# Kernel tuning notes

Hardware: AMD Instinct MI355X
Metric: run time of the kernel (lower is better)

## Reference

```python
import jax, jax.numpy as jnp
import numpy as np

CHUNK = 64
EPS = 1e-5


def segsum(a):
    # a: (..., T) -> (..., T, T) lower-triangular cumulative segment sums; -inf above diag
    T = a.shape[-1]
    cs = jnp.cumsum(a, axis=-1)
    ss = cs[..., :, None] - cs[..., None, :]
    mask = jnp.tril(jnp.ones((T, T), dtype=bool))
    return jnp.where(mask, ss, -jnp.inf)


def ssd(x, A, B, C, chunk):
    # x: (b, L, h, p), A: (b, L, h), B/C: (b, L, n)
    b, L, h, p = x.shape
    c = L // chunk
    x = x.reshape(b, c, chunk, h, p)
    A = A.reshape(b, c, chunk, h).transpose(0, 3, 1, 2)          # b h c l
    B = B.reshape(b, c, chunk, -1)                               # b c l n
    C = C.reshape(b, c, chunk, -1)                               # b c l n
    A_cum = jnp.cumsum(A, axis=-1)                               # b h c l
    Lmat = jnp.exp(segsum(A))                                    # b h c l l (causal decay)
    # intra-chunk (diagonal-block) output
    Y_diag = jnp.einsum('bcln,bcsn,bhcls,bcshp->bclhp', C, B, Lmat, x)
    # per-chunk states
    decay_states = jnp.exp(A_cum[..., -1:] - A_cum)              # b h c l
    states = jnp.einsum('bcln,bhcl,bclhp->bchpn', B, decay_states, x)
    states = jnp.concatenate([jnp.zeros_like(states[:, :1]), states], axis=1)  # b (c+1) h p n
    # inter-chunk recurrence via chunk-level segsum
    A_last = jnp.pad(A_cum[..., -1], ((0, 0), (0, 0), (1, 0)))   # b h (c+1)
    decay_chunk = jnp.exp(segsum(A_last))                        # b h (c+1) (c+1)
    new_states = jnp.einsum('bhzc,bchpn->bzhpn', decay_chunk, states)
    states, final = new_states[:, :-1], new_states[:, -1:]
    Y_off = jnp.einsum('bcln,bchpn,bhcl->bclhp', C, states, jnp.exp(A_cum))
    return (Y_diag + Y_off).reshape(b, L, h, p), final


def mamba2(x, W_in, conv_w, conv_b, dt_bias, A_log, D, norm_w, W_out):
    d_inner = norm_w.shape[0]
    nheads = dt_bias.shape[0]
    d_state = (conv_b.shape[0] - d_inner) // 2
    headdim = d_inner // nheads
    k_conv = conv_w.shape[0]
    b, L, _ = x.shape

    zxbcdt = x @ W_in                                            # (b, L, 2*d_inner+2*n+h)
    z = zxbcdt[..., :d_inner]
    xBC = zxbcdt[..., d_inner:2 * d_inner + 2 * d_state]
    dt = jax.nn.softplus(zxbcdt[..., 2 * d_inner + 2 * d_state:] + dt_bias)  # (b, L, h)
    A = -jnp.exp(A_log)                                          # (h,)

    # causal depthwise conv (zero init conv state == left-pad k_conv-1 zeros) + silu
    xp = jnp.pad(xBC, ((0, 0), (k_conv - 1, 0), (0, 0)))
    xBC = jax.lax.conv_general_dilated(
        xp, conv_w, (1,), 'VALID',
        dimension_numbers=('NWC', 'WIO', 'NWC'),
        feature_group_count=conv_b.shape[0])
    xBC = jax.nn.silu(xBC + conv_b)

    xs = xBC[..., :d_inner].reshape(b, L, nheads, headdim)       # (b, L, h, p)
    Bm = xBC[..., d_inner:d_inner + d_state]                     # (b, L, n)
    Cm = xBC[..., d_inner + d_state:]                            # (b, L, n)

    Y, _ = ssd(xs * dt[..., None], A * dt, Bm, Cm, CHUNK)
    Y = Y + xs * D                                               # D: (h, 1) broadcasts over p
    y = Y.reshape(b, L, d_inner)

    # gated RMSNorm
    y = y * jax.nn.silu(z)
    y = y * jax.lax.rsqrt(jnp.mean(y * y, axis=-1, keepdims=True) + EPS) * norm_w
    return y @ W_out


def setup_inputs():
    key = jax.random.key(0)
    ks = jax.random.split(key, 8)
    B, L, d_model = 2, 4096, 1024
    expand, d_state, k_conv, headdim = 2, 128, 4, 64
    d_inner = expand * d_model
    nheads = d_inner // headdim
    d_in_proj = 2 * d_inner + 2 * d_state + nheads
    conv_dim = d_inner + 2 * d_state
    return {
        'x': jax.random.normal(ks[0], (B, L, d_model), jnp.float32),
        'W_in': jax.random.normal(ks[1], (d_model, d_in_proj), jnp.float32) / np.sqrt(d_model).astype(np.float32),
        'conv_w': jax.random.normal(ks[2], (k_conv, 1, conv_dim), jnp.float32) / np.sqrt(k_conv).astype(np.float32),
        'conv_b': jnp.zeros((conv_dim,), jnp.float32),
        'dt_bias': jax.random.normal(ks[3], (nheads,), jnp.float32) * 0.5 - 2.0,
        'A_log': jnp.log(1.0 + 15.0 * jax.random.uniform(ks[4], (nheads,), jnp.float32)),
        'D': jax.random.normal(ks[5], (nheads, 1), jnp.float32),
        'norm_w': jnp.ones((d_inner,), jnp.float32),
        'W_out': jax.random.normal(ks[6], (d_inner, d_model), jnp.float32) / np.sqrt(d_inner).astype(np.float32),
    }


def reference(x, W_in, conv_w, conv_b, dt_bias, A_log, D, norm_w, W_out):
    return mamba2(x, W_in, conv_w, conv_b, dt_bias, A_log, D, norm_w, W_out)
```

## Files before the change

kernel.cpp:

```cpp
#include <hip/hip_runtime.h>
#include <hip/hip_fp16.h>

typedef _Float16 f16;
typedef _Float16 f16x4 __attribute__((ext_vector_type(4)));
typedef _Float16 f16x8 __attribute__((ext_vector_type(8)));
typedef float f32x4 __attribute__((ext_vector_type(4)));

#define DEV __device__ __forceinline__

constexpr int BB    = 2;
constexpr int LL    = 4096;
constexpr int DM    = 1024;
constexpr int DIN   = 2048;
constexpr int DST   = 128;
constexpr int NH    = 32;
constexpr int HD    = 64;
constexpr int NC    = 64;
constexpr int MROWS = BB * LL;
constexpr int NPROJ = 2*DIN + 2*DST + NH;
constexpr int NZ    = 2*DIN + 2*DST;
constexpr int CONVD = DIN + 2*DST;
constexpr int DT_OFF = 2*DIN + 2*DST;
constexpr int BOFF  = DIN;
constexpr int COFF  = DIN + DST;

DEV float silu_f(float v) { return v / (1.f + __expf(-v)); }

DEV void gload_lds16(const f16* gsrc, f16* lds_dst) {
  __builtin_amdgcn_global_load_lds(
      (const __attribute__((address_space(1))) void*)gsrc,
      (__attribute__((address_space(3))) void*)lds_dst, 16, 0, 0);
}

__global__ __launch_bounds__(256)
void tof16_kernel(const float* __restrict__ src, f16* __restrict__ dst, int n8) {
  int i = blockIdx.x * 256 + threadIdx.x;
  if (i >= n8) return;
  f32x4 a = *(const f32x4*)(src + (size_t)i*8);
  f32x4 b = *(const f32x4*)(src + (size_t)i*8 + 4);
  f16x8 o;
#pragma unroll
  for (int j = 0; j < 4; ++j) { o[j] = (f16)a[j]; o[4+j] = (f16)b[j]; }
  *(f16x8*)(dst + (size_t)i*8) = o;
}

__global__ __launch_bounds__(256)
void transpose_f32_to_f16(const float* __restrict__ src, f16* __restrict__ dst,
                          int K, int N, int srcLd) {
  __shared__ float tbuf[32][33];
  int n0 = blockIdx.x * 32, k0 = blockIdx.y * 32;
  int tx = threadIdx.x & 31, ty = threadIdx.x >> 5;
  for (int i = ty; i < 32; i += 8)
    tbuf[i][tx] = src[(size_t)(k0 + i)*srcLd + n0 + tx];
  __syncthreads();
  for (int i = ty; i < 32; i += 8)
    dst[(size_t)(n0 + i)*K + (k0 + tx)] = (f16)tbuf[tx][i];
}

template<bool C16>
__global__ __launch_bounds__(256)
void gemm_lds(const f16* __restrict__ A, const f16* __restrict__ Bt,
              void* __restrict__ Cp, int M, int N, int K, int ldc) {
  __shared__ f16 As[128*64];
  __shared__ f16 Bs[128*64];
  int nbn = N >> 7;
  int bm = blockIdx.x / nbn, bn = blockIdx.x % nbn;
  const int tid  = threadIdx.x;
  const int wave = tid >> 6, lane = tid & 63;
  const int lrow = lane & 15;
  const int kgrp = lane >> 4;
  const int wr = wave >> 1, wc = wave & 1;
  const int srow = lane >> 3;
  const int scol = (lane & 7) * 8;
  const f16* Abase = A  + (size_t)(bm*128 + srow)*K + scol;
  const f16* Bbase = Bt + (size_t)(bn*128 + srow)*K + scol;

  f32x4 acc[4][4] = {};

  for (int k0 = 0; k0 < K; k0 += 64) {
    __syncthreads();
#pragma unroll
    for (int i = 0; i < 4; ++i) {
      int seg = wave*4 + i;
      gload_lds16(Abase + (size_t)seg*8*K + k0, As + seg*512);
      gload_lds16(Bbase + (size_t)seg*8*K + k0, Bs + seg*512);
    }
    __syncthreads();
#pragma unroll
    for (int kk = 0; kk < 64; kk += 32) {
      f16x8 af[4], bfr[4];
#pragma unroll
      for (int m = 0; m < 4; ++m)
        af[m] = *(const f16x8*)(As + (wr*64 + m*16 + lrow)*64 + kk + kgrp*8);
#pragma unroll
      for (int n = 0; n < 4; ++n)
        bfr[n] = *(const f16x8*)(Bs + (wc*64 + n*16 + lrow)*64 + kk + kgrp*8);
#pragma unroll
      for (int m = 0; m < 4; ++m)
#pragma unroll
        for (int n = 0; n < 4; ++n)
          acc[m][n] = __builtin_amdgcn_mfma_f32_16x16x32_f16(af[m], bfr[n], acc[m][n], 0, 0, 0);
    }
  }
  int crow0 = bm*128 + wr*64, ccol0 = bn*128 + wc*64;
#pragma unroll
  for (int m = 0; m < 4; ++m)
#pragma unroll
    for (int n = 0; n < 4; ++n) {
      int r0 = crow0 + m*16 + (lane >> 4)*4;
      int c0 = ccol0 + n*16 + (lane & 15);
#pragma unroll
      for (int r = 0; r < 4; ++r) {
        if constexpr (C16) {
          f16* C = (f16*)Cp;
          C[(size_t)(r0 + r)*ldc + c0] = (f16)acc[m][n][r];
        } else {
          float* C = (float*)Cp;
          C[(size_t)(r0 + r)*ldc + c0] = acc[m][n][r];
        }
      }
    }
}

__global__ __launch_bounds__(256)
void dt_kernel(const float* __restrict__ x, const float* __restrict__ Win,
               const float* __restrict__ dt_bias, float* __restrict__ dt) {
  __shared__ float xs[64][132];
  __shared__ float ws[128][32];
  int r0 = blockIdx.x * 64;
  int t = threadIdx.x;
  int r = t >> 2, c0 = (t & 3) * 8;
  float acc[8] = {};
  for (int kt = 0; kt < 1024; kt += 128) {
    __syncthreads();
#pragma unroll
    for (int i = 0; i < 8; ++i) {
      int idx4 = t + i*256;
      int rr = idx4 >> 5, c4 = (idx4 & 31) * 4;
      *(f32x4*)&xs[rr][c4] = *(const f32x4*)(x + (size_t)(r0 + rr)*1024 + kt + c4);
    }
#pragma unroll
    for (int i = 0; i < 4; ++i) {
      int idx4 = t + i*256;
      int rr = idx4 >> 3, c4 = (idx4 & 7) * 4;
      *(f32x4*)&ws[rr][c4] = *(const f32x4*)(Win + (size_t)(kt + rr)*NPROJ + DT_OFF + c4);
    }
    __syncthreads();
#pragma unroll 8
    for (int k = 0; k < 128; ++k) {
      float xv = xs[r][k];
      f32x4 w0 = *(const f32x4*)&ws[k][c0];
      f32x4 w1 = *(const f32x4*)&ws[k][c0 + 4];
#pragma unroll
      for (int j = 0; j < 4; ++j) { acc[j] += xv * w0[j]; acc[4+j] += xv * w1[j]; }
    }
  }
#pragma unroll
  for (int j = 0; j < 8; ++j) {
    float v = acc[j] + dt_bias[c0 + j];
    float sp = (v > 20.f) ? v : log1pf(__expf(v));
    dt[(size_t)(r0 + r)*NH + c0 + j] = sp;
  }
}

__global__ __launch_bounds__(256)
void conv_kernel(const f16* __restrict__ zxh, const float* __restrict__ cw,
                 const float* __restrict__ cb, f16* __restrict__ out) {
  int i = blockIdx.x * 256 + threadIdx.x;
  int row = i / (CONVD/8);
  int c8  = (i - row*(CONVD/8)) * 8;
  int lb = row & (LL - 1);
  f32x4 a0 = *(const f32x4*)(cb + c8);
  f32x4 a1 = *(const f32x4*)(cb + c8 + 4);
#pragma unroll
  for (int j = 0; j < 4; ++j) {
    int lsrc = lb - 3 + j;
    if (lsrc >= 0) {
      f16x8 v = *(const f16x8*)(zxh + (size_t)(row - 3 + j)*NZ + BOFF + c8);
      f32x4 w0 = *(const f32x4*)(cw + j*CONVD + c8);
      f32x4 w1 = *(const f32x4*)(cw + j*CONVD + c8 + 4);
#pragma unroll
      for (int jj = 0; jj < 4; ++jj) {
        a0[jj] += (float)v[jj]   * w0[jj];
        a1[jj] += (float)v[4+jj] * w1[jj];
      }
    }
  }
  f16x8 o;
#pragma unroll
  for (int jj = 0; jj < 4; ++jj) {
    o[jj]   = (f16)silu_f(a0[jj]);
    o[4+jj] = (f16)silu_f(a1[jj]);
  }
  *(f16x8*)(out + (size_t)row*CONVD + c8) = o;
}

__global__ __launch_bounds__(256)
void acum_kernel(const float* __restrict__ dt, const float* __restrict__ A_log,
                 float* __restrict__ Acum) {
  int bc = blockIdx.x;
  int wave = threadIdx.x >> 6, lane = threadIdx.x & 63;
  int row = bc*64 + lane;
  for (int hh = 0; hh < 8; ++hh) {
    int h = wave*8 + hh;
    float A = -__expf(A_log[h]);
    float v = A * dt[(size_t)row*NH + h];
#pragma unroll
    for (int off = 1; off < 64; off <<= 1) {
      float u = __shfl_up(v, off);
      if (lane >= off) v += u;
    }
    Acum[((size_t)bc*NH + h)*64 + lane] = v;
  }
}

__global__ __launch_bounds__(256)
void gbuf_kernel(const f16* __restrict__ xbc, f16* __restrict__ G) {
  __shared__ float Cs[64][128];
  __shared__ float Bsm[64][128];
  int bc = blockIdx.x;
  int row0 = bc * 64;
  int t = threadIdx.x;
#pragma unroll
  for (int i = 0; i < 4; ++i) {
    int idx = t + i*256;
    int r = idx >> 4, c8 = (idx & 15) * 8;
    f16x8 cv = *(const f16x8*)(xbc + (size_t)(row0 + r)*CONVD + COFF + c8);
    f16x8 bv = *(const f16x8*)(xbc + (size_t)(row0 + r)*CONVD + BOFF + c8);
    f32x4 c0v = {(float)cv[0], (float)cv[1], (float)cv[2], (float)cv[3]};
    f32x4 c1v = {(float)cv[4], (float)cv[5], (float)cv[6], (float)cv[7]};
    f32x4 b0v = {(float)bv[0], (float)bv[1], (float)bv[2], (float)bv[3]};
    f32x4 b1v = {(float)bv[4], (float)bv[5], (float)bv[6], (float)bv[7]};
    *(f32x4*)&Cs[r][c8]      = c0v;  *(f32x4*)&Cs[r][c8 + 4]  = c1v;
    *(f32x4*)&Bsm[r][c8]     = b0v;  *(f32x4*)&Bsm[r][c8 + 4] = b1v;
  }
  __syncthreads();
  int l0 = (t >> 4)*4, s0 = (t & 15)*4;
  float acc[4][4] = {};
  for (int n4 = 0; n4 < 128; n4 += 4) {
    f32x4 cv[4], bv[4];
#pragma unroll
    for (int i = 0; i < 4; ++i) cv[i] = *(const f32x4*)&Cs[l0 + i][n4];
#pragma unroll
    for (int j = 0; j < 4; ++j) bv[j] = *(const f32x4*)&Bsm[s0 + j][n4];
#pragma unroll
    for (int i = 0; i < 4; ++i)
#pragma unroll
      for (int j = 0; j < 4; ++j)
        acc[i][j] += cv[i][0]*bv[j][0] + cv[i][1]*bv[j][1] + cv[i][2]*bv[j][2] + cv[i][3]*bv[j][3];
  }
#pragma unroll
  for (int i = 0; i < 4; ++i) {
    f16x4 v = {(f16)acc[i][0], (f16)acc[i][1], (f16)acc[i][2], (f16)acc[i][3]};
    *(f16x4*)(G + ((size_t)bc*64 + l0 + i)*64 + s0) = v;
  }
}

__global__ __launch_bounds__(256)
void ssd_a_kernel(const f16* __restrict__ xbc, const float* __restrict__ dtb,
                  const f16* __restrict__ Gg, const float* __restrict__ Acum,
                  f16* __restrict__ Ybuf, f16* __restrict__ states) {
  __shared__ union {
    struct { f16 XdT[64][72]; f16 Gt[64][72]; f16 BT[128][72]; } s;
    float Yl[64][68];
    float Sl[64][132];
  } u;
  __shared__ float ac[64], dts[64];
  int bc = blockIdx.x >> 5, h = blockIdx.x & 31;
  int row0 = bc*64, t = threadIdx.x;
  if (t < 64) {
    ac[t]  = Acum[((size_t)bc*NH + h)*64 + t];
    dts[t] = dtb[(size_t)(row0 + t)*NH + h];
  }
  __syncthreads();
  float ac63 = ac[63];
#pragma unroll
  for (int i = 0; i < 2; ++i) {
    int idx = t + i*256; int l = idx >> 3, p8 = (idx & 7)*8;
    f16x8 v = *(const f16x8*)(xbc + (size_t)(row0 + l)*CONVD + h*HD + p8);
    float d = dts[l];
#pragma unroll
    for (int j = 0; j < 8; ++j) u.s.XdT[p8 + j][l] = (f16)((float)v[j]*d);
  }
#pragma unroll
  for (int i = 0; i < 4; ++i) {
    int idx = t + i*256; int l = idx >> 4, n8 = (idx & 15)*8;
    f16x8 v = *(const f16x8*)(xbc + (size_t)(row0 + l)*CONVD + BOFF + n8);
    float dl = __expf(ac63 - ac[l]);
#pragma unroll
    for (int j = 0; j < 8; ++j) u.s.BT[n8 + j][l] = (f16)((float)v[j]*dl);
  }
#pragma unroll
  for (int i = 0; i < 2; ++i) {
    int idx = t + i*256; int l = idx >> 3, s8 = (idx & 7)*8;
    f16x8 g = *(const f16x8*)(Gg + (size_t)bc*4096 + l*64 + s8);
    float al = ac[l];
    f16x8 o;
#pragma unroll
    for (int j = 0; j < 8; ++j) {
      int s = s8 + j;
      o[j] = (l >= s) ? (f16)((float)g[j] * __expf(al - ac[s])) : (f16)0.f;
    }
    *(f16x8*)&u.s.Gt[l][s8] = o;
  }
  __syncthreads();
  int wave = t >> 6, lane = t & 63;
  int lrow = lane & 15, kgrp = lane >> 4;
  f32x4 yacc[4] = {};
  f32x4 sacc[8] = {};
#pragma unroll
  for (int kk = 0; kk < 64; kk += 32) {
    f16x8 afy = *(const f16x8*)&u.s.Gt[wave*16 + lrow][kk + kgrp*8];
    f16x8 afs = *(const f16x8*)&u.s.XdT[wave*16 + lrow][kk + kgrp*8];
#pragma unroll
    for (int n = 0; n < 4; ++n) {
      f16x8 bf = *(const f16x8*)&u.s.XdT[n*16 + lrow][kk + kgrp*8];
      yacc[n] = __builtin_amdgcn_mfma_f32_16x16x32_f16(afy, bf, yacc[n], 0, 0, 0);
    }
#pragma unroll
    for (int n = 0; n < 8; ++n) {
      f16x8 bf = *(const f16x8*)&u.s.BT[n*16 + lrow][kk + kgrp*8];
      sacc[n] = __builtin_amdgcn_mfma_f32_16x16x32_f16(afs, bf, sacc[n], 0, 0, 0);
    }
  }
  __syncthreads();
#pragma unroll
  for (int n = 0; n < 4; ++n)
#pragma unroll
    for (int r = 0; r < 4; ++r)
      u.Yl[wave*16 + kgrp*4 + r][n*16 + lrow] = yacc[n][r];
  __syncthreads();
#pragma unroll
  for (int i = 0; i < 2; ++i) {
    int idx = t + i*256; int l = idx >> 3, p8 = (idx & 7)*8;
    f16x8 o;
#pragma unroll
    for (int j = 0; j < 8; ++j) o[j] = (f16)u.Yl[l][p8 + j];
    *(f16x8*)(Ybuf + (size_t)(row0 + l)*DIN + h*HD + p8) = o;
  }
  __syncthreads();
#pragma unroll
  for (int n = 0; n < 8; ++n)
#pragma unroll
    for (int r = 0; r < 4; ++r)
      u.Sl[wave*16 + kgrp*4 + r][n*16 + lrow] = sacc[n][r];
  __syncthreads();
  size_t sb = ((size_t)bc*NH + h)*8192;
#pragma unroll
  for (int i = 0; i < 4; ++i) {
    int idx = t + i*256; int p = idx >> 4, n8 = (idx & 15)*8;
    f16x8 o;
#pragma unroll
    for (int j = 0; j < 8; ++j) o[j] = (f16)u.Sl[p][n8 + j];
    *(f16x8*)(states + sb + (size_t)p*128 + n8) = o;
  }
}

__global__ __launch_bounds__(256)
void scan_kernel(f16* __restrict__ states, const float* __restrict__ Acum) {
  int bid = blockIdx.x;
  int bh = bid >> 3, pgrp = bid & 7;
  int b = bh >> 5, h = bh & 31;
  int t = threadIdx.x;
  int p = pgrp*8 + (t >> 5), n4 = (t & 31) * 4;
  size_t off = (size_t)p*128 + n4;
  f32x4 carry = {0.f, 0.f, 0.f, 0.f};
  for (int c = 0; c < NC; ++c) {
    size_t base = ((size_t)(b*NC + c)*NH + h)*8192;
    f16x4 cv = *(f16x4*)(states + base + off);
    f16x4 st;
#pragma unroll
    for (int j = 0; j < 4; ++j) st[j] = (f16)carry[j];
    *(f16x4*)(states + base + off) = st;
    float tc = __expf(Acum[((size_t)(b*NC + c)*NH + h)*64 + 63]);
#pragma unroll
    for (int j = 0; j < 4; ++j) carry[j] = carry[j]*tc + (float)cv[j];
  }
}

__global__ __launch_bounds__(256)
void yoff_kernel(const f16* __restrict__ xbc, const f16* __restrict__ zxh,
                 const f16* __restrict__ states, const float* __restrict__ Acum,
                 const float* __restrict__ Dp, f16* __restrict__ Ybuf) {
  __shared__ union {
    struct { f16 Ch[64][136]; f16 Sin[64][136]; } s;
    float Yl[64][68];
  } u;
  __shared__ float eac[64];
  int bc = blockIdx.x >> 5, h = blockIdx.x & 31;
  int row0 = bc*64, t = threadIdx.x;
  if (t < 64) eac[t] = __expf(Acum[((size_t)bc*NH + h)*64 + t]);
  size_t sb = ((size_t)bc*NH + h)*8192;
#pragma unroll
  for (int i = 0; i < 4; ++i) {
    int idx = t + i*256; int r = idx >> 4, c8 = (idx & 15)*8;
    *(f16x8*)&u.s.Ch[r][c8]  = *(const f16x8*)(xbc + (size_t)(row0 + r)*CONVD + COFF + c8);
    *(f16x8*)&u.s.Sin[r][c8] = *(const f16x8*)(states + sb + (size_t)r*128 + c8);
  }
  __syncthreads();
  int wave = t >> 6, lane = t & 63;
  int lrow = lane & 15, kgrp = lane >> 4;
  f32x4 acc[4] = {};
#pragma unroll
  for (int kk = 0; kk < 128; kk += 32) {
    f16x8 af = *(const f16x8*)&u.s.Ch[wave*16 + lrow][kk + kgrp*8];
#pragma unroll
    for (int n = 0; n < 4; ++n) {
      f16x8 bf = *(const f16x8*)&u.s.Sin[n*16 + lrow][kk + kgrp*8];
      acc[n] = __builtin_amdgcn_mfma_f32_16x16x32_f16(af, bf, acc[n], 0, 0, 0);
    }
  }
  __syncthreads();
#pragma unroll
  for (int n = 0; n < 4; ++n)
#pragma unroll
    for (int r = 0; r < 4; ++r)
      u.Yl[wave*16 + kgrp*4 + r][n*16 + lrow] = acc[n][r];
  __syncthreads();
  float Dh = Dp[h];
#pragma unroll
  for (int i = 0; i < 2; ++i) {
    int idx = t + i*256; int l = idx >> 3, p8 = (idx & 7)*8;
    int row = row0 + l;
    f16x8 yd = *(const f16x8*)(Ybuf + (size_t)row*DIN + h*HD + p8);
    f16x8 zh = *(const f16x8*)(zxh + (size_t)row*NZ + h*HD + p8);
    f16x8 xs = *(const f16x8*)(xbc + (size_t)row*CONVD + h*HD + p8);
    float e = eac[l];
    f16x8 o;
#pragma unroll
    for (int j = 0; j < 8; ++j) {
      float yv = (float)yd[j] + e*u.Yl[l][p8 + j] + (float)xs[j]*Dh;
      o[j] = (f16)(yv * silu_f((float)zh[j]));
    }
    *(f16x8*)(Ybuf + (size_t)row*DIN + h*HD + p8) = o;
  }
}

__global__ __launch_bounds__(256)
void rms_kernel(const f16* __restrict__ yg, const float* __restrict__ nw,
                f16* __restrict__ yh) {
  __shared__ float red[4];
  int row = blockIdx.x, t = threadIdx.x;
  f16x8 v = *(const f16x8*)(yg + (size_t)row*DIN + t*8);
  float f[8];
  float ss = 0.f;
#pragma unroll
  for (int j = 0; j < 8; ++j) { f[j] = (float)v[j]; ss += f[j]*f[j]; }
#pragma unroll
  for (int off = 32; off > 0; off >>= 1) ss += __shfl_down(ss, off);
  if ((t & 63) == 0) red[t >> 6] = ss;
  __syncthreads();
  float tot = red[0] + red[1] + red[2] + red[3];
  float sc = rsqrtf(tot * (1.f/2048.f) + 1e-5f);
  f32x4 w0 = *(const f32x4*)(nw + t*8);
  f32x4 w1 = *(const f32x4*)(nw + t*8 + 4);
  f16x8 o;
#pragma unroll
  for (int j = 0; j < 4; ++j) {
    o[j]   = (f16)(f[j]   * sc * w0[j]);
    o[4+j] = (f16)(f[4+j] * sc * w1[j]);
  }
  *(f16x8*)(yh + (size_t)row*DIN + t*8) = o;
}

extern "C" void kernel_launch(void* const* d_in, const int* in_sizes, int n_in,
                              void* d_out, int out_size, void* d_ws, size_t ws_size,
                              hipStream_t stream) {
  const float* x       = (const float*)d_in[0];
  const float* W_in    = (const float*)d_in[1];
  const float* conv_w  = (const float*)d_in[2];
  const float* conv_b  = (const float*)d_in[3];
  const float* dt_bias = (const float*)d_in[4];
  const float* A_log   = (const float*)d_in[5];
  const float* Dp      = (const float*)d_in[6];
  const float* norm_w  = (const float*)d_in[7];
  const float* W_out   = (const float*)d_in[8];

  constexpr size_t WS_NEED = 213909504;
  if (ws_size < WS_NEED) return;

  char* w = (char*)d_ws;
  f16*   states = (f16*)(w + 0);
  f16*   winT   = (f16*)(w + 0);
  f16*   yh     = (f16*)(w + 0);
  f16*   xh     = (f16*)(w + 33554432);
  f16*   woutT  = (f16*)(w + 33554432);
  f16*   zxh    = (f16*)(w + 67108864);
  f16*   xbcc   = (f16*)(w + 138412032);
  f16*   Ybuf   = (f16*)(w + 176160768);
  float* dtb    = (float*)(w + 209715200);
  float* Acum   = (float*)(w + 210763776);
  f16*   Gg     = (f16*)(w + 211812352);

  tof16_kernel<<<4096, 256, 0, stream>>>(x, xh, MROWS*DM/8);
  transpose_f32_to_f16<<<dim3(NZ/32, DM/32), 256, 0, stream>>>(W_in, winT, DM, NZ, NPROJ);
  gemm_lds<true><<<(MROWS/128)*(NZ/128), 256, 0, stream>>>(xh, winT, zxh, MROWS, NZ, DM, NZ);
  dt_kernel<<<MROWS/64, 256, 0, stream>>>(x, W_in, dt_bias, dtb);
  conv_kernel<<<MROWS*(CONVD/8)/256, 256, 0, stream>>>(zxh, conv_w, conv_b, xbcc);
  acum_kernel<<<BB*NC, 256, 0, stream>>>(dtb, A_log, Acum);
  gbuf_kernel<<<BB*NC, 256, 0, stream>>>(xbcc, Gg);
  ssd_a_kernel<<<BB*NC*NH, 256, 0, stream>>>(xbcc, dtb, Gg, Acum, Ybuf, states);
  scan_kernel<<<BB*NH*8, 256, 0, stream>>>(states, Acum);
  yoff_kernel<<<BB*NC*NH, 256, 0, stream>>>(xbcc, zxh, states, Acum, Dp, Ybuf);
  transpose_f32_to_f16<<<dim3(DM/32, DIN/32), 256, 0, stream>>>(W_out, woutT, DIN, DM, DM);
  rms_kernel<<<MROWS, 256, 0, stream>>>(Ybuf, norm_w, yh);
  gemm_lds<false><<<(MROWS/128)*(DM/128), 256, 0, stream>>>(yh, woutT, d_out, MROWS, DM, DIN, DM);
}
```

Before: 438.6 us.

## Replace GEMM with triple-buffered 256x128 tile pipelined LDS kernel

Both projection GEMMs move to a new kernel with 512 threads and 256x128 output tiles. It uses a K-step of 32 and a three-stage LDS ring, so global-to-LDS loads for tile t+2 are in flight while MFMAs run on tile t. The old two-barrier-per-iteration scheme becomes explicit vmcnt waits plus a single barrier. The aim is to hide global load latency and get more reuse per block, at the cost of more LDS per block and fewer blocks in the grid.

Result: no change. 436.2 us (-0.5%).

```diff
diff --git a/kernel.cpp b/kernel.cpp
--- a/kernel.cpp
+++ b/kernel.cpp
@@ -58,51 +58,69 @@
 }
 
 template<bool C16>
-__global__ __launch_bounds__(256)
-void gemm_lds(const f16* __restrict__ A, const f16* __restrict__ Bt,
-              void* __restrict__ Cp, int M, int N, int K, int ldc) {
-  __shared__ f16 As[128*64];
-  __shared__ f16 Bs[128*64];
-  int nbn = N >> 7;
-  int bm = blockIdx.x / nbn, bn = blockIdx.x % nbn;
+__global__ __launch_bounds__(512, 2)
+void gemm_p(const f16* __restrict__ A, const f16* __restrict__ Bt,
+            void* __restrict__ Cp, int M, int N, int K, int ldc) {
+  __shared__ f16 As3[3][256*32];
+  __shared__ f16 Bs3[3][128*32];
+  const int nbn = N >> 7;
+  const int bm = blockIdx.x / nbn, bn = blockIdx.x % nbn;
   const int tid  = threadIdx.x;
   const int wave = tid >> 6, lane = tid & 63;
-  const int lrow = lane & 15;
-  const int kgrp = lane >> 4;
-  const int wr = wave >> 1, wc = wave & 1;
-  const int srow = lane >> 3;
-  const int scol = (lane & 7) * 8;
-  const f16* Abase = A  + (size_t)(bm*128 + srow)*K + scol;
-  const f16* Bbase = Bt + (size_t)(bn*128 + srow)*K + scol;
+  const int lrow = lane & 15, kgrp = lane >> 4;
+  const int wm = wave >> 1, wn = wave & 1;
+  const int nt = K >> 5;
+
+  const int rS = tid >> 2;
+  const int cS = (tid & 3) * 8;
+  const f16* Ag = A  + (size_t)(bm*256 + rS)*K + cS;
+  const f16* Bg = Bt + (size_t)(bn*128 + rS)*K + cS;
+  const int ldsOff = wave * 512;
 
   f32x4 acc[4][4] = {};
 
-  for (int k0 = 0; k0 < K; k0 += 64) {
-    __syncthreads();
-#pragma unroll
-    for (int i = 0; i < 4; ++i) {
-      int seg = wave*4 + i;
-      gload_lds16(Abase + (size_t)seg*8*K + k0, As + seg*512);
-      gload_lds16(Bbase + (size_t)seg*8*K + k0, Bs + seg*512);
-    }
-    __syncthreads();
-#pragma unroll
-    for (int kk = 0; kk < 64; kk += 32) {
-      f16x8 af[4], bfr[4];
-#pragma unroll
-      for (int m = 0; m < 4; ++m)
-        af[m] = *(const f16x8*)(As + (wr*64 + m*16 + lrow)*64 + kk + kgrp*8);
+  auto STAGE = [&](int buf, int t) {
+    const f16* a0 = Ag + (size_t)t*32;
+    gload_lds16(a0,                 As3[buf] + ldsOff);
+    gload_lds16(a0 + (size_t)128*K, As3[buf] + ldsOff + 4096);
+    gload_lds16(Bg + (size_t)t*32,  Bs3[buf] + ldsOff);
+  };
+
+  STAGE(0, 0);
+  if (nt > 1) {
+    STAGE(1, 1);
+    asm volatile("s_waitcnt vmcnt(3)" ::: "memory");
+  } else {
+    asm volatile("s_waitcnt vmcnt(0)" ::: "memory");
+  }
+  __builtin_amdgcn_s_barrier();
+  __builtin_amdgcn_sched_barrier(0);
+
+  for (int t = 0; t < nt; ++t) {
+    const int cur = t % 3;
+    if (t + 2 < nt) STAGE((t + 2) % 3, t + 2);
+    const f16* Ab = As3[cur];
+    const f16* Bb = Bs3[cur];
+    f16x8 bf[4];
+#pragma unroll
+    for (int n = 0; n < 4; ++n)
+      bf[n] = *(const f16x8*)(Bb + (wn*64 + n*16 + lrow)*32 + kgrp*8);
+#pragma unroll
+    for (int m = 0; m < 4; ++m) {
+      f16x8 af = *(const f16x8*)(Ab + (wm*64 + m*16 + lrow)*32 + kgrp*8);
 #pragma unroll
       for (int n = 0; n < 4; ++n)
-        bfr[n] = *(const f16x8*)(Bs + (wc*64 + n*16 + lrow)*64 + kk + kgrp*8);
-#pragma unroll
-      for (int m = 0; m < 4; ++m)
-#pragma unroll
-        for (int n = 0; n < 4; ++n)
-          acc[m][n] = __builtin_amdgcn_mfma_f32_16x16x32_f16(af[m], bfr[n], acc[m][n], 0, 0, 0);
-    }
-  }
-  int crow0 = bm*128 + wr*64, ccol0 = bn*128 + wc*64;
+        acc[m][n] = __builtin_amdgcn_mfma_f32_16x16x32_f16(af, bf[n], acc[m][n], 0, 0, 0);
+    }
+    if (t + 1 < nt) {
+      if (t + 2 < nt) asm volatile("s_waitcnt vmcnt(3)" ::: "memory");
+      else            asm volatile("s_waitcnt vmcnt(0)" ::: "memory");
+      __builtin_amdgcn_s_barrier();
+      __builtin_amdgcn_sched_barrier(0);
+    }
+  }
+
+  int crow0 = bm*256 + wm*64, ccol0 = bn*128 + wn*64;
 #pragma unroll
   for (int m = 0; m < 4; ++m)
 #pragma unroll
@@ -494,7 +512,7 @@
 
   tof16_kernel<<<4096, 256, 0, stream>>>(x, xh, MROWS*DM/8);
   transpose_f32_to_f16<<<dim3(NZ/32, DM/32), 256, 0, stream>>>(W_in, winT, DM, NZ, NPROJ);
-  gemm_lds<true><<<(MROWS/128)*(NZ/128), 256, 0, stream>>>(xh, winT, zxh, MROWS, NZ, DM, NZ);
+  gemm_p<true><<<(MROWS/256)*(NZ/128), 512, 0, stream>>>(xh, winT, zxh, MROWS, NZ, DM, NZ);
   dt_kernel<<<MROWS/64, 256, 0, stream>>>(x, W_in, dt_bias, dtb);
   conv_kernel<<<MROWS*(CONVD/8)/256, 256, 0, stream>>>(zxh, conv_w, conv_b, xbcc);
   acum_kernel<<<BB*NC, 256, 0, stream>>>(dtb, A_log, Acum);
@@ -504,5 +522,5 @@
   yoff_kernel<<<BB*NC*NH, 256, 0, stream>>>(xbcc, zxh, states, Acum, Dp, Ybuf);
   transpose_f32_to_f16<<<dim3(DM/32, DIN/32), 256, 0, stream>>>(W_out, woutT, DIN, DM, DM);
   rms_kernel<<<MROWS, 256, 0, stream>>>(Ybuf, norm_w, yh);
-  gemm_lds<false><<<(MROWS/128)*(DM/128), 256, 0, stream>>>(yh, woutT, d_out, MROWS, DM, DIN, DM);
-}
+  gemm_p<false><<<(MROWS/256)*(DM/128), 512, 0, stream>>>(yh, woutT, d_out, MROWS, DM, DIN, DM);
+}
```
